# Kernel tuning notes

Hardware: AMD Instinct MI355X
Metric: run time of the kernel (lower is better)

## Reference

```python
import jax, jax.numpy as jnp
import numpy as np

N, D, E = 100000, 128, 600000  # nodes, channels, edges per subgraph


def _cos(a, b, eps=1e-8):
    # torch.nn.functional.cosine_similarity semantics (norm clamped at eps)
    na = jnp.maximum(jnp.linalg.norm(a, axis=-1), eps)
    nb = jnp.maximum(jnp.linalg.norm(b, axis=-1), eps)
    return jnp.sum(a * b, axis=-1) / (na * nb)


def _get_edge_att(x, edge_index, edge_attr):
    # utils.get_edge_att (source unavailable): edge weight modulated by
    # endpoint-feature cosine similarity.
    return edge_attr * _cos(x[edge_index[0]], x[edge_index[1]])


def _cgat(x, edge_index, edge_attr, node_mask, W, b):
    m = node_mask[:, None]
    h = jnp.where(m, x @ W.T, x)                       # lin only on masked nodes
    msg = edge_attr[:, None] * h[edge_index[0]]        # [E, D]
    ssum = jax.ops.segment_sum(msg, edge_index[1], num_segments=N)
    cnt = jax.ops.segment_sum(jnp.ones_like(edge_attr), edge_index[1], num_segments=N)
    mean = ssum / jnp.maximum(cnt, 1.0)[:, None]       # safe mean (0 for isolated nodes)
    out = jnp.where(m, mean, 0.0) + h                  # aggr only written at masked nodes
    return jnp.where(m, jax.nn.sigmoid(out + b), out)


def setup_inputs() -> dict:
    key = jax.random.key(0)
    ks = jax.random.split(key, 10)
    x = jax.random.normal(ks[0], (N, D), jnp.float32)
    edge_index_ii = jax.random.randint(ks[1], (2, E), 0, N)
    edge_attr_ii = jax.random.uniform(ks[2], (E,), jnp.float32)
    edge_index_uiu = jax.random.randint(ks[3], (2, E), 0, N)
    edge_attr_uiu = jax.random.uniform(ks[4], (E,), jnp.float32)
    node_mask_item = jnp.arange(N) < (N * 8 // 10)
    s = 1.0 / np.sqrt(D)  # torch Linear default init range
    W1_ii = jax.random.uniform(ks[5], (D, D), jnp.float32, -s, s)
    W2_ii = jax.random.uniform(ks[6], (D, D), jnp.float32, -s, s)
    W_uiu = jax.random.uniform(ks[7], (D, D), jnp.float32, -s, s)
    z = jnp.zeros((D,), jnp.float32)  # bias zero-initialized in reset_parameters
    return {
        "x": x,
        "edge_attr_ii": edge_attr_ii,
        "edge_attr_uiu": edge_attr_uiu,
        "W1_ii": W1_ii, "b1_ii": z, "W2_ii": W2_ii, "b2_ii": z,
        "W_uiu": W_uiu, "b_uiu": z,
        "edge_index_ii": edge_index_ii,
        "edge_index_uiu": edge_index_uiu,
        "node_mask_item": node_mask_item,
    }


def reference(x, edge_attr_ii, edge_attr_uiu, W1_ii, b1_ii, W2_ii, b2_ii,
              W_uiu, b_uiu, edge_index_ii, edge_index_uiu, node_mask_item):
    # item-item graph
    ea1 = _get_edge_att(x, edge_index_ii, edge_attr_ii)
    x1 = _cgat(x, edge_index_ii, ea1, node_mask_item, W1_ii, b1_ii)
    ea2 = _get_edge_att(x1, edge_index_ii, edge_attr_ii)
    x2 = _cgat(x1, edge_index_ii, ea2, node_mask_item, W2_ii, b2_ii)
    # user-item graph (cgat1_uiu applied twice in the source)
    all_mask = jnp.ones((N,), bool)
    u1 = _cgat(x2, edge_index_uiu, edge_attr_uiu, all_mask, W_uiu, b_uiu)
    u2 = _cgat(u1, edge_index_uiu, edge_attr_uiu, all_mask, W_uiu, b_uiu)
    # edge predictions on the uiu edges (the only nonzero part of edge_y_pred)
    return _cos(u2[edge_index_uiu[0]], u2[edge_index_uiu[1]])
```

## Files before the change

kernel.cpp:

```cpp
#include <hip/hip_runtime.h>
#include <cstdint>
#include <cmath>

#define D 128
#define SCAN_BS 1024

typedef __attribute__((ext_vector_type(8))) short bf16x8;
typedef __attribute__((ext_vector_type(4))) float f32x4;

__device__ __forceinline__ unsigned short f2b(float f) {
    unsigned u = __float_as_uint(f);
    return (unsigned short)((u + 0x7FFFu + ((u >> 16) & 1u)) >> 16);
}
__device__ __forceinline__ unsigned pack2(float a, float b) {
    return (unsigned)f2b(a) | ((unsigned)f2b(b) << 16);
}
__device__ __forceinline__ float blo(unsigned u) { return __uint_as_float(u << 16); }
__device__ __forceinline__ float bhi(unsigned u) { return __uint_as_float(u & 0xffff0000u); }
__device__ __forceinline__ int swzbyte(int row, int b) {
    return (row << 8) + (b ^ ((row & 7) << 4));
}

__device__ __forceinline__ unsigned fp8pk4(float a, float b, float c, float d) {
    int w = __builtin_amdgcn_cvt_pk_fp8_f32(a, b, 0, false);
    w = __builtin_amdgcn_cvt_pk_fp8_f32(c, d, w, true);
    return (unsigned)w;
}
__device__ __forceinline__ unsigned char fp8one(float v) {
    return (unsigned char)(__builtin_amdgcn_cvt_pk_fp8_f32(v, v, 0, false) & 0xff);
}
__device__ __forceinline__ void fp8up8(uint2 w, float* f) {
    auto l0 = __builtin_amdgcn_cvt_pk_f32_fp8((int)w.x, false);
    auto h0 = __builtin_amdgcn_cvt_pk_f32_fp8((int)w.x, true);
    auto l1 = __builtin_amdgcn_cvt_pk_f32_fp8((int)w.y, false);
    auto h1 = __builtin_amdgcn_cvt_pk_f32_fp8((int)w.y, true);
    f[0] = l0[0]; f[1] = l0[1]; f[2] = h0[0]; f[3] = h0[1];
    f[4] = l1[0]; f[5] = l1[1]; f[6] = h1[0]; f[7] = h1[1];
}

__global__ void mask_canon_kernel(const unsigned char* __restrict__ mraw,
                                  int* __restrict__ mout, int n) {
    int i = blockIdx.x * blockDim.x + threadIdx.x;
    if (i >= n) return;
    bool isbool = (mraw[1] | mraw[2] | mraw[3]) != 0;
    int v;
    if (isbool) v = (mraw[i] != 0);
    else        v = (((const int*)mraw)[i] != 0);
    mout[i] = v;
}

__global__ void conv_norm_kernel(const float* __restrict__ x,
                                 unsigned short* __restrict__ xb,
                                 unsigned char* __restrict__ xn8, int n) {
    int t = blockIdx.x * blockDim.x + threadIdx.x;
    int i = t >> 4, sl = t & 15;
    if (i >= n) return;
    unsigned rid = ((unsigned)i << 4) | (unsigned)sl;
    const float4* ip = (const float4*)(x + (size_t)i * D) + sl * 2;
    float4 a = ip[0], b = ip[1];
    float f[8] = {a.x, a.y, a.z, a.w, b.x, b.y, b.z, b.w};
    float acc = 0.f;
    #pragma unroll
    for (int q = 0; q < 8; q++) acc += f[q] * f[q];
    #pragma unroll
    for (int o = 8; o; o >>= 1) acc += __shfl_xor(acc, o);
    float r = 1.0f / fmaxf(sqrtf(acc), 1e-8f);
    uint4 ob;
    #pragma unroll
    for (int q = 0; q < 4; q++) (&ob.x)[q] = pack2(f[2*q], f[2*q+1]);
    ((uint4*)xb)[rid] = ob;
    uint2 o8;
    o8.x = fp8pk4(f[0]*r, f[1]*r, f[2]*r, f[3]*r);
    o8.y = fp8pk4(f[4]*r, f[5]*r, f[6]*r, f[7]*r);
    ((uint2*)xn8)[rid] = o8;
}

__global__ void w3_to_b16_kernel(const float* __restrict__ W1, const float* __restrict__ W2,
                                 const float* __restrict__ Wu,
                                 unsigned short* __restrict__ o1, unsigned short* __restrict__ o2,
                                 unsigned short* __restrict__ ou) {
    int t = blockIdx.x * blockDim.x + threadIdx.x;
    const float* src; unsigned short* dst; int b;
    if (t < 2048)      { src = W1; dst = o1; b = t; }
    else if (t < 4096) { src = W2; dst = o2; b = t - 2048; }
    else               { src = Wu; dst = ou; b = t - 4096; }
    const float4* ip = (const float4*)src + (size_t)b * 2;
    float4 a = ip[0], c = ip[1];
    uint4 o;
    o.x = pack2(a.x, a.y); o.y = pack2(a.z, a.w);
    o.z = pack2(c.x, c.y); o.w = pack2(c.z, c.w);
    ((uint4*)dst)[b] = o;
}

__global__ void count_pos2_kernel(const int* __restrict__ dstA, const int* __restrict__ dstB,
                                  int* __restrict__ tmp2, int* __restrict__ posw,
                                  int n, int e_total) {
    int t = blockIdx.x * blockDim.x + threadIdx.x;
    if (t >= 2 * e_total) return;
    int g = (t >= e_total);
    int e = t - g * e_total;
    int d = (g ? dstB : dstA)[e];
    posw[t] = atomicAdd(&tmp2[(size_t)g * n + d], 1);
}

__global__ __launch_bounds__(SCAN_BS)
void scan_block_kernel(const int* __restrict__ deg2, int* __restrict__ off2,
                       int* __restrict__ bsum2, int n) {
    __shared__ int s[SCAN_BS];
    int g = blockIdx.y;
    int gid = blockIdx.x * SCAN_BS + threadIdx.x;
    int v = (gid < n) ? deg2[(size_t)g * n + gid] : 0;
    s[threadIdx.x] = v;
    __syncthreads();
    for (int o = 1; o < SCAN_BS; o <<= 1) {
        int t = (threadIdx.x >= o) ? s[threadIdx.x - o] : 0;
        __syncthreads();
        s[threadIdx.x] += t;
        __syncthreads();
    }
    if (gid < n) off2[(size_t)g * (n + 1) + gid] = s[threadIdx.x] - v;
    if (threadIdx.x == SCAN_BS - 1) bsum2[g * 256 + blockIdx.x] = s[SCAN_BS - 1];
}

__global__ void scan_bsum_kernel(int* __restrict__ bsum2, int nb) {
    __shared__ int s[256];
    int g = blockIdx.y;
    int v = ((int)threadIdx.x < nb) ? bsum2[g * 256 + threadIdx.x] : 0;
    s[threadIdx.x] = v;
    __syncthreads();
    for (int o = 1; o < 256; o <<= 1) {
        int t = (threadIdx.x >= o) ? s[threadIdx.x - o] : 0;
        __syncthreads();
        s[threadIdx.x] += t;
        __syncthreads();
    }
    if ((int)threadIdx.x < nb) bsum2[g * 256 + threadIdx.x] = s[threadIdx.x] - v;
}

__global__ __launch_bounds__(SCAN_BS)
void add_offsets_kernel(int* __restrict__ off2, const int* __restrict__ bsum2,
                        int n, int e_total) {
    int g = blockIdx.y;
    int gid = blockIdx.x * SCAN_BS + threadIdx.x;
    if (gid < n) off2[(size_t)g * (n + 1) + gid] += bsum2[g * 256 + blockIdx.x];
    if (gid == 0) off2[(size_t)g * (n + 1) + n] = e_total;
}

__global__ void scatter_edges2_kernel(const int* __restrict__ srcA, const int* __restrict__ dstA,
                                      const float* __restrict__ aA,
                                      const int* __restrict__ srcB, const int* __restrict__ dstB,
                                      const float* __restrict__ aB,
                                      const int* __restrict__ off2, const int* __restrict__ posw,
                                      int2* __restrict__ edaA, int2* __restrict__ edaB,
                                      int n, int e_total) {
    int t = blockIdx.x * blockDim.x + threadIdx.x;
    if (t >= 2 * e_total) return;
    int g = (t >= e_total);
    int e = t - g * e_total;
    int d = (g ? dstB : dstA)[e];
    int p = off2[(size_t)g * (n + 1) + d] + posw[t];
    int2 rec;
    rec.x = (g ? srcB : srcA)[e];
    rec.y = __float_as_int((g ? aB : aA)[e]);
    (g ? edaB : edaA)[p] = rec;
}

__global__ __launch_bounds__(512)
void gemm_mfma_kernel(const unsigned short* __restrict__ xb,
                      const unsigned short* __restrict__ Wb,
                      const int* __restrict__ mask,
                      unsigned short* __restrict__ hb,
                      unsigned char* __restrict__ hb8, int n) {
    __shared__ char sXb[128 * 256];
    __shared__ char sWb[128 * 256];
    const int tid = threadIdx.x;
    const int blockRow0 = blockIdx.x * 128;

    const uint4* xg = (const uint4*)xb + (size_t)blockRow0 * 16;
    #pragma unroll
    for (int it = 0; it < 4; it++) {
        int f = tid + it * 512;
        int row = f >> 4, kc = f & 15;
        uint4 v = make_uint4(0, 0, 0, 0);
        if (blockRow0 + row < n) v = xg[f];
        *(uint4*)(sXb + swzbyte(row, kc * 16)) = v;
    }
    const uint4* wg = (const uint4*)Wb;
    #pragma unroll
    for (int it = 0; it < 4; it++) {
        int f = tid + it * 512;
        int row = f >> 4, kc = f & 15;
        *(uint4*)(sWb + swzbyte(row, kc * 16)) = wg[f];
    }
    __syncthreads();

    const int wid = tid >> 6, lane = tid & 63;
    const int lrow = lane & 15, kg = lane >> 4;
    f32x4 acc[8];
    #pragma unroll
    for (int j = 0; j < 8; j++) acc[j] = (f32x4)(0.f);

    const int arow = wid * 16 + lrow;
    #pragma unroll
    for (int kk = 0; kk < 4; kk++) {
        int kb = kk * 64 + kg * 16;
        bf16x8 af = *(const bf16x8*)(sXb + swzbyte(arow, kb));
        #pragma unroll
        for (int j = 0; j < 8; j++) {
            bf16x8 bfr = *(const bf16x8*)(sWb + swzbyte(j * 16 + lrow, kb));
            acc[j] = __builtin_amdgcn_mfma_f32_16x16x32_bf16(af, bfr, acc[j], 0, 0, 0);
        }
    }

    const int growbase = blockRow0 + wid * 16 + kg * 4;
    const int lrbase = wid * 16 + kg * 4;
    #pragma unroll
    for (int r = 0; r < 4; r++) {
        int row = growbase + r;
        if (row >= n) continue;
        bool pm = mask ? (mask[row] != 0) : true;
        int lr = lrbase + r;
        #pragma unroll
        for (int j = 0; j < 8; j++) {
            int col = j * 16 + lrow;
            float v;
            if (pm) v = acc[j][r];
            else    v = blo((unsigned)*(const unsigned short*)(sXb + (lr << 8) + ((2 * col) ^ ((lr & 7) << 4))));
            hb [(size_t)row * D + col] = f2b(v);
            hb8[(size_t)row * D + col] = fp8one(v);
        }
    }
}

__global__ __launch_bounds__(256)
void fused_agg_kernel(const unsigned short* __restrict__ hb,
                      const unsigned char* __restrict__ hb8,
                      const unsigned char* __restrict__ xn8,
                      const int2* __restrict__ eda,
                      const int* __restrict__ off,
                      const float* __restrict__ bias, const int* __restrict__ mask,
                      unsigned short* __restrict__ outb,
                      unsigned char* __restrict__ xnout8, int n) {
    int t = blockIdx.x * blockDim.x + threadIdx.x;
    int i = t >> 4, sl = t & 15;
    if (i >= n) return;
    const uint2* h8 = (const uint2*)hb8;
    const uint2* x8 = (const uint2*)xn8;
    unsigned rid = ((unsigned)i << 4) | (unsigned)sl;
    uint4 hv = ((const uint4*)hb)[rid];
    bool m = mask ? (mask[i] != 0) : true;

    float fo[8];
    if (!m) {
        #pragma unroll
        for (int q = 0; q < 4; q++) {
            unsigned u = (&hv.x)[q];
            fo[2*q] = blo(u); fo[2*q+1] = bhi(u);
        }
    } else {
        float xd[8];
        if (xn8) fp8up8(x8[rid], xd);

        int s0 = off[i], s1 = off[i + 1];
        float acc[8];
        #pragma unroll
        for (int k = 0; k < 8; k++) acc[k] = 0.f;

        int p = s0;
        while (p + 2 <= s1) {
            int2 e0 = eda[p], e1 = eda[p + 1];
            unsigned r0 = ((unsigned)e0.x << 4) | (unsigned)sl;
            unsigned r1 = ((unsigned)e1.x << 4) | (unsigned)sl;
            uint2 g0 = h8[r0], g1 = h8[r1];
            float c0 = __int_as_float(e0.y), c1 = __int_as_float(e1.y);
            if (xn8) {
                float xs0[8], xs1[8];
                fp8up8(x8[r0], xs0);
                fp8up8(x8[r1], xs1);
                float pr0 = 0.f, pr1 = 0.f;
                #pragma unroll
                for (int k = 0; k < 8; k++) {
                    pr0 += xs0[k] * xd[k];
                    pr1 += xs1[k] * xd[k];
                }
                #pragma unroll
                for (int o = 8; o; o >>= 1) {
                    pr0 += __shfl_xor(pr0, o);
                    pr1 += __shfl_xor(pr1, o);
                }
                c0 *= pr0; c1 *= pr1;
            }
            float f0[8], f1[8];
            fp8up8(g0, f0);
            fp8up8(g1, f1);
            #pragma unroll
            for (int k = 0; k < 8; k++) acc[k] += c0 * f0[k] + c1 * f1[k];
            p += 2;
        }
        if (p < s1) {
            int2 e0 = eda[p];
            unsigned r0 = ((unsigned)e0.x << 4) | (unsigned)sl;
            uint2 g0 = h8[r0];
            float c0 = __int_as_float(e0.y);
            if (xn8) {
                float xs0[8];
                fp8up8(x8[r0], xs0);
                float pr0 = 0.f;
                #pragma unroll
                for (int k = 0; k < 8; k++) pr0 += xs0[k] * xd[k];
                #pragma unroll
                for (int o = 8; o; o >>= 1) pr0 += __shfl_xor(pr0, o);
                c0 *= pr0;
            }
            float f0[8];
            fp8up8(g0, f0);
            #pragma unroll
            for (int k = 0; k < 8; k++) acc[k] += c0 * f0[k];
        }

        float inv = 1.0f / fmaxf((float)(s1 - s0), 1.0f);
        const float4* bp = (const float4*)(bias + 8 * sl);
        float4 bv0 = bp[0], bv1 = bp[1];
        float bb[8] = {bv0.x, bv0.y, bv0.z, bv0.w, bv1.x, bv1.y, bv1.z, bv1.w};
        #pragma unroll
        for (int q = 0; q < 4; q++) {
            unsigned u = (&hv.x)[q];
            float z0 = acc[2*q]   * inv + blo(u) + bb[2*q];
            float z1 = acc[2*q+1] * inv + bhi(u) + bb[2*q+1];
            fo[2*q]   = 1.0f / (1.0f + __expf(-z0));
            fo[2*q+1] = 1.0f / (1.0f + __expf(-z1));
        }
    }

    uint4 o;
    #pragma unroll
    for (int q = 0; q < 4; q++) (&o.x)[q] = pack2(fo[2*q], fo[2*q+1]);
    ((uint4*)outb)[rid] = o;

    if (xnout8) {
        float ss = 0.f;
        #pragma unroll
        for (int k = 0; k < 8; k++) ss += fo[k] * fo[k];
        #pragma unroll
        for (int o2 = 8; o2; o2 >>= 1) ss += __shfl_xor(ss, o2);
        float r = 1.0f / fmaxf(sqrtf(ss), 1e-8f);
        uint2 on;
        on.x = fp8pk4(fo[0]*r, fo[1]*r, fo[2]*r, fo[3]*r);
        on.y = fp8pk4(fo[4]*r, fo[5]*r, fo[6]*r, fo[7]*r);
        ((uint2*)xnout8)[rid] = on;
    }
}

__global__ void edge_cos_b16_kernel(const unsigned short* __restrict__ xb,
                                    const int* __restrict__ src,
                                    const int* __restrict__ dst,
                                    float* __restrict__ out, int e_total) {
    int t = blockIdx.x * blockDim.x + threadIdx.x;
    int e = t >> 4, lane = t & 15;
    if (e >= e_total) return;
    int s = src[e], d = dst[e];
    uint4 a = ((const uint4*)xb)[((unsigned)s << 4) | lane];
    uint4 b = ((const uint4*)xb)[((unsigned)d << 4) | lane];
    float sd = 0.f, ss = 0.f, dd = 0.f;
    #pragma unroll
    for (int q = 0; q < 4; q++) {
        unsigned ua = (&a.x)[q], ub = (&b.x)[q];
        float a0 = blo(ua), a1 = bhi(ua), b0 = blo(ub), b1 = bhi(ub);
        sd += a0 * b0 + a1 * b1;
        ss += a0 * a0 + a1 * a1;
        dd += b0 * b0 + b1 * b1;
    }
    #pragma unroll
    for (int o = 8; o; o >>= 1) {
        sd += __shfl_xor(sd, o, 16);
        ss += __shfl_xor(ss, o, 16);
        dd += __shfl_xor(dd, o, 16);
    }
    if (lane == 0) {
        float rs = 1.0f / fmaxf(sqrtf(ss), 1e-8f);
        float rd = 1.0f / fmaxf(sqrtf(dd), 1e-8f);
        out[e] = sd * rs * rd;
    }
}

extern "C" void kernel_launch(void* const* d_in, const int* in_sizes, int n_in,
                              void* d_out, int out_size, void* d_ws, size_t ws_size,
                              hipStream_t stream) {
    const float* x        = (const float*)d_in[0];
    const float* attr_ii  = (const float*)d_in[1];
    const float* attr_uiu = (const float*)d_in[2];
    const float* W1       = (const float*)d_in[3];
    const float* b1       = (const float*)d_in[4];
    const float* W2       = (const float*)d_in[5];
    const float* b2       = (const float*)d_in[6];
    const float* Wu       = (const float*)d_in[7];
    const float* bu       = (const float*)d_in[8];
    const int*   ei_ii    = (const int*)d_in[9];
    const int*   ei_uiu   = (const int*)d_in[10];
    const unsigned char* mraw = (const unsigned char*)d_in[11];

    const int n = in_sizes[0] / D;
    const int e = in_sizes[1];
    const size_t ND = (size_t)n * D;

    unsigned short* Ab  = (unsigned short*)d_ws;
    unsigned short* Bb0 = Ab + ND;
    unsigned short* Bb1 = Bb0 + ND;
    unsigned short* Wb1 = Bb1 + ND;
    unsigned short* Wb2 = Wb1 + 16384;
    unsigned short* Wbu = Wb2 + 16384;
    unsigned char* Ab8  = (unsigned char*)(Wbu + 16384);
    unsigned char* Xn80 = Ab8 + ND;
    unsigned char* Xn81 = Xn80 + ND;
    int2* eda_ii  = (int2*)(Xn81 + ND);
    int2* eda_uiu = eda_ii + e;
    int* maskI    = (int*)(eda_uiu + e);
    int* tmp2     = maskI + n;
    int* bsum2    = tmp2 + 2 * (size_t)n;
    int* off2     = bsum2 + 512;
    int* off_ii   = off2;
    int* off_uiu  = off2 + (n + 1);
    int* posw     = (int*)Ab;

    const int* src_ii  = ei_ii,  * dst_ii  = ei_ii + e;
    const int* src_uiu = ei_uiu, * dst_uiu = ei_uiu + e;
    float* out = (float*)d_out;

    const int nb = (n + SCAN_BS - 1) / SCAN_BS;
    const int gN16 = ((size_t)n * 16 + 255) / 256;
    const int gE16 = ((size_t)e * 16 + 255) / 256;
    const int gGemm = (n + 127) / 128;

    mask_canon_kernel<<<(n + 255) / 256, 256, 0, stream>>>(mraw, maskI, n);

    hipMemsetAsync(tmp2, 0, 2 * (size_t)n * sizeof(int), stream);
    count_pos2_kernel<<<(2 * e + 255) / 256, 256, 0, stream>>>(dst_ii, dst_uiu, tmp2, posw, n, e);
    scan_block_kernel<<<dim3(nb, 2), SCAN_BS, 0, stream>>>(tmp2, off2, bsum2, n);
    scan_bsum_kernel<<<dim3(1, 2), 256, 0, stream>>>(bsum2, nb);
    add_offsets_kernel<<<dim3(nb, 2), SCAN_BS, 0, stream>>>(off2, bsum2, n, e);
    scatter_edges2_kernel<<<(2 * e + 255) / 256, 256, 0, stream>>>(
        src_ii, dst_ii, attr_ii, src_uiu, dst_uiu, attr_uiu, off2, posw, eda_ii, eda_uiu, n, e);

    conv_norm_kernel<<<gN16, 256, 0, stream>>>(x, Bb0, Xn80, n);
    w3_to_b16_kernel<<<24, 256, 0, stream>>>(W1, W2, Wu, Wb1, Wb2, Wbu);

    gemm_mfma_kernel<<<gGemm, 512, 0, stream>>>(Bb0, Wb1, maskI, Ab, Ab8, n);
    fused_agg_kernel<<<gN16, 256, 0, stream>>>(Ab, Ab8, Xn80, eda_ii, off_ii, b1, maskI, Bb1, Xn81, n);

    gemm_mfma_kernel<<<gGemm, 512, 0, stream>>>(Bb1, Wb2, maskI, Ab, Ab8, n);
    fused_agg_kernel<<<gN16, 256, 0, stream>>>(Ab, Ab8, Xn81, eda_ii, off_ii, b2, maskI, Bb0, nullptr, n);

    gemm_mfma_kernel<<<gGemm, 512, 0, stream>>>(Bb0, Wbu, nullptr, Ab, Ab8, n);
    fused_agg_kernel<<<gN16, 256, 0, stream>>>(Ab, Ab8, nullptr, eda_uiu, off_uiu, bu, nullptr, Bb1, nullptr, n);

    gemm_mfma_kernel<<<gGemm, 512, 0, stream>>>(Bb1, Wbu, nullptr, Ab, Ab8, n);
    fused_agg_kernel<<<gN16, 256, 0, stream>>>(Ab, Ab8, nullptr, eda_uiu, off_uiu, bu, nullptr, Bb0, nullptr, n);

    edge_cos_b16_kernel<<<gE16, 256, 0, stream>>>(Bb0, src_uiu, dst_uiu, out, e);
}
```

Before: 351.9 us.

## Interleave fp8 h and normalized-x rows; fuse mask/memset into conversion kernel

Stores the fp8 transformed features and the fp8 normalized features in one interleaved 256-byte row per node. A gathered source edge then fetches both from adjacent cache lines instead of two separate arrays. The mask canonicalization, the counter memset and the fp32-to-bf16 conversion are merged into one kernel, which removes two launches. The interleaved layout doubles the stride for the uiu layers, where only the h half is read, so gather locality may suffer there.

```diff
diff --git a/kernel.cpp b/kernel.cpp
--- a/kernel.cpp
+++ b/kernel.cpp
@@ -38,24 +38,20 @@
     f[4] = l1[0]; f[5] = l1[1]; f[6] = h1[0]; f[7] = h1[1];
 }
 
-__global__ void mask_canon_kernel(const unsigned char* __restrict__ mraw,
-                                  int* __restrict__ mout, int n) {
-    int i = blockIdx.x * blockDim.x + threadIdx.x;
-    if (i >= n) return;
-    bool isbool = (mraw[1] | mraw[2] | mraw[3]) != 0;
-    int v;
-    if (isbool) v = (mraw[i] != 0);
-    else        v = (((const int*)mraw)[i] != 0);
-    mout[i] = v;
-}
-
-__global__ void conv_norm_kernel(const float* __restrict__ x,
-                                 unsigned short* __restrict__ xb,
-                                 unsigned char* __restrict__ xn8, int n) {
-    int t = blockIdx.x * blockDim.x + threadIdx.x;
+__global__ void conv_mask_zero_kernel(const float* __restrict__ x,
+                                      const unsigned char* __restrict__ mraw,
+                                      unsigned short* __restrict__ xb,
+                                      unsigned char* __restrict__ pk,
+                                      int* __restrict__ maskI,
+                                      int* __restrict__ tmp2, int n) {
+    int t = blockIdx.x * blockDim.x + threadIdx.x;
+    if (t < 2 * n) tmp2[t] = 0;
+    if (t < n) {
+        bool isbool = (mraw[1] | mraw[2] | mraw[3]) != 0;
+        maskI[t] = isbool ? (mraw[t] != 0) : (((const int*)mraw)[t] != 0);
+    }
     int i = t >> 4, sl = t & 15;
     if (i >= n) return;
-    unsigned rid = ((unsigned)i << 4) | (unsigned)sl;
     const float4* ip = (const float4*)(x + (size_t)i * D) + sl * 2;
     float4 a = ip[0], b = ip[1];
     float f[8] = {a.x, a.y, a.z, a.w, b.x, b.y, b.z, b.w};
@@ -68,11 +64,11 @@
     uint4 ob;
     #pragma unroll
     for (int q = 0; q < 4; q++) (&ob.x)[q] = pack2(f[2*q], f[2*q+1]);
-    ((uint4*)xb)[rid] = ob;
+    ((uint4*)xb)[((unsigned)i << 4) | (unsigned)sl] = ob;
     uint2 o8;
     o8.x = fp8pk4(f[0]*r, f[1]*r, f[2]*r, f[3]*r);
     o8.y = fp8pk4(f[4]*r, f[5]*r, f[6]*r, f[7]*r);
-    ((uint2*)xn8)[rid] = o8;
+    ((uint2*)pk)[(unsigned)i * 32u + 16u + (unsigned)sl] = o8;
 }
 
 __global__ void w3_to_b16_kernel(const float* __restrict__ W1, const float* __restrict__ W2,
@@ -170,7 +166,7 @@
                       const unsigned short* __restrict__ Wb,
                       const int* __restrict__ mask,
                       unsigned short* __restrict__ hb,
-                      unsigned char* __restrict__ hb8, int n) {
+                      unsigned char* __restrict__ pk, int n) {
     __shared__ char sXb[128 * 256];
     __shared__ char sWb[128 * 256];
     const int tid = threadIdx.x;
@@ -226,26 +222,25 @@
             float v;
             if (pm) v = acc[j][r];
             else    v = blo((unsigned)*(const unsigned short*)(sXb + (lr << 8) + ((2 * col) ^ ((lr & 7) << 4))));
-            hb [(size_t)row * D + col] = f2b(v);
-            hb8[(size_t)row * D + col] = fp8one(v);
+            hb[(size_t)row * D + col] = f2b(v);
+            pk[(size_t)row * 256 + col] = fp8one(v);
         }
     }
 }
 
 __global__ __launch_bounds__(256)
 void fused_agg_kernel(const unsigned short* __restrict__ hb,
-                      const unsigned char* __restrict__ hb8,
-                      const unsigned char* __restrict__ xn8,
+                      const unsigned char* __restrict__ pk,
+                      const int usecos,
                       const int2* __restrict__ eda,
                       const int* __restrict__ off,
                       const float* __restrict__ bias, const int* __restrict__ mask,
                       unsigned short* __restrict__ outb,
-                      unsigned char* __restrict__ xnout8, int n) {
+                      unsigned char* __restrict__ pknext, int n) {
     int t = blockIdx.x * blockDim.x + threadIdx.x;
     int i = t >> 4, sl = t & 15;
     if (i >= n) return;
-    const uint2* h8 = (const uint2*)hb8;
-    const uint2* x8 = (const uint2*)xn8;
+    const uint2* p2 = (const uint2*)pk;
     unsigned rid = ((unsigned)i << 4) | (unsigned)sl;
     uint4 hv = ((const uint4*)hb)[rid];
     bool m = mask ? (mask[i] != 0) : true;
@@ -259,7 +254,7 @@
         }
     } else {
         float xd[8];
-        if (xn8) fp8up8(x8[rid], xd);
+        if (usecos) fp8up8(p2[(unsigned)i * 32u + 16u + (unsigned)sl], xd);
 
         int s0 = off[i], s1 = off[i + 1];
         float acc[8];
@@ -269,14 +264,14 @@
         int p = s0;
         while (p + 2 <= s1) {
             int2 e0 = eda[p], e1 = eda[p + 1];
-            unsigned r0 = ((unsigned)e0.x << 4) | (unsigned)sl;
-            unsigned r1 = ((unsigned)e1.x << 4) | (unsigned)sl;
-            uint2 g0 = h8[r0], g1 = h8[r1];
+            unsigned r0 = (unsigned)e0.x * 32u + (unsigned)sl;
+            unsigned r1 = (unsigned)e1.x * 32u + (unsigned)sl;
+            uint2 g0 = p2[r0], g1 = p2[r1];
             float c0 = __int_as_float(e0.y), c1 = __int_as_float(e1.y);
-            if (xn8) {
+            if (usecos) {
                 float xs0[8], xs1[8];
-                fp8up8(x8[r0], xs0);
-                fp8up8(x8[r1], xs1);
+                fp8up8(p2[r0 + 16u], xs0);
+                fp8up8(p2[r1 + 16u], xs1);
                 float pr0 = 0.f, pr1 = 0.f;
                 #pragma unroll
                 for (int k = 0; k < 8; k++) {
@@ -299,12 +294,12 @@
         }
         if (p < s1) {
             int2 e0 = eda[p];
-            unsigned r0 = ((unsigned)e0.x << 4) | (unsigned)sl;
-            uint2 g0 = h8[r0];
+            unsigned r0 = (unsigned)e0.x * 32u + (unsigned)sl;
+            uint2 g0 = p2[r0];
             float c0 = __int_as_float(e0.y);
-            if (xn8) {
+            if (usecos) {
                 float xs0[8];
-                fp8up8(x8[r0], xs0);
+                fp8up8(p2[r0 + 16u], xs0);
                 float pr0 = 0.f;
                 #pragma unroll
                 for (int k = 0; k < 8; k++) pr0 += xs0[k] * xd[k];
@@ -337,7 +332,7 @@
     for (int q = 0; q < 4; q++) (&o.x)[q] = pack2(fo[2*q], fo[2*q+1]);
     ((uint4*)outb)[rid] = o;
 
-    if (xnout8) {
+    if (pknext) {
         float ss = 0.f;
         #pragma unroll
         for (int k = 0; k < 8; k++) ss += fo[k] * fo[k];
@@ -347,7 +342,7 @@
         uint2 on;
         on.x = fp8pk4(fo[0]*r, fo[1]*r, fo[2]*r, fo[3]*r);
         on.y = fp8pk4(fo[4]*r, fo[5]*r, fo[6]*r, fo[7]*r);
-        ((uint2*)xnout8)[rid] = on;
+        ((uint2*)pknext)[(unsigned)i * 32u + 16u + (unsigned)sl] = on;
     }
 }
 
@@ -409,10 +404,9 @@
     unsigned short* Wb1 = Bb1 + ND;
     unsigned short* Wb2 = Wb1 + 16384;
     unsigned short* Wbu = Wb2 + 16384;
-    unsigned char* Ab8  = (unsigned char*)(Wbu + 16384);
-    unsigned char* Xn80 = Ab8 + ND;
-    unsigned char* Xn81 = Xn80 + ND;
-    int2* eda_ii  = (int2*)(Xn81 + ND);
+    unsigned char* PK0 = (unsigned char*)(Wbu + 16384);
+    unsigned char* PK1 = PK0 + 2 * ND;
+    int2* eda_ii  = (int2*)(PK1 + 2 * ND);
     int2* eda_uiu = eda_ii + e;
     int* maskI    = (int*)(eda_uiu + e);
     int* tmp2     = maskI + n;
@@ -431,9 +425,8 @@
     const int gE16 = ((size_t)e * 16 + 255) / 256;
     const int gGemm = (n + 127) / 128;
 
-    mask_canon_kernel<<<(n + 255) / 256, 256, 0, stream>>>(mraw, maskI, n);
-
-    hipMemsetAsync(tmp2, 0, 2 * (size_t)n * sizeof(int), stream);
+    conv_mask_zero_kernel<<<gN16, 256, 0, stream>>>(x, mraw, Bb0, PK0, maskI, tmp2, n);
+
     count_pos2_kernel<<<(2 * e + 255) / 256, 256, 0, stream>>>(dst_ii, dst_uiu, tmp2, posw, n, e);
     scan_block_kernel<<<dim3(nb, 2), SCAN_BS, 0, stream>>>(tmp2, off2, bsum2, n);
     scan_bsum_kernel<<<dim3(1, 2), 256, 0, stream>>>(bsum2, nb);
@@ -441,20 +434,19 @@
     scatter_edges2_kernel<<<(2 * e + 255) / 256, 256, 0, stream>>>(
         src_ii, dst_ii, attr_ii, src_uiu, dst_uiu, attr_uiu, off2, posw, eda_ii, eda_uiu, n, e);
 
-    conv_norm_kernel<<<gN16, 256, 0, stream>>>(x, Bb0, Xn80, n);
     w3_to_b16_kernel<<<24, 256, 0, stream>>>(W1, W2, Wu, Wb1, Wb2, Wbu);
 
-    gemm_mfma_kernel<<<gGemm, 512, 0, stream>>>(Bb0, Wb1, maskI, Ab, Ab8, n);
-    fused_agg_kernel<<<gN16, 256, 0, stream>>>(Ab, Ab8, Xn80, eda_ii, off_ii, b1, maskI, Bb1, Xn81, n);
-
-    gemm_mfma_kernel<<<gGemm, 512, 0, stream>>>(Bb1, Wb2, maskI, Ab, Ab8, n);
-    fused_agg_kernel<<<gN16, 256, 0, stream>>>(Ab, Ab8, Xn81, eda_ii, off_ii, b2, maskI, Bb0, nullptr, n);
-
-    gemm_mfma_kernel<<<gGemm, 512, 0, stream>>>(Bb0, Wbu, nullptr, Ab, Ab8, n);
-    fused_agg_kernel<<<gN16, 256, 0, stream>>>(Ab, Ab8, nullptr, eda_uiu, off_uiu, bu, nullptr, Bb1, nullptr, n);
-
-    gemm_mfma_kernel<<<gGemm, 512, 0, stream>>>(Bb1, Wbu, nullptr, Ab, Ab8, n);
-    fused_agg_kernel<<<gN16, 256, 0, stream>>>(Ab, Ab8, nullptr, eda_uiu, off_uiu, bu, nullptr, Bb0, nullptr, n);
+    gemm_mfma_kernel<<<gGemm, 512, 0, stream>>>(Bb0, Wb1, maskI, Ab, PK0, n);
+    fused_agg_kernel<<<gN16, 256, 0, stream>>>(Ab, PK0, 1, eda_ii, off_ii, b1, maskI, Bb1, PK1, n);
+
+    gemm_mfma_kernel<<<gGemm, 512, 0, stream>>>(Bb1, Wb2, maskI, Ab, PK1, n);
+    fused_agg_kernel<<<gN16, 256, 0, stream>>>(Ab, PK1, 1, eda_ii, off_ii, b2, maskI, Bb0, nullptr, n);
+
+    gemm_mfma_kernel<<<gGemm, 512, 0, stream>>>(Bb0, Wbu, nullptr, Ab, PK0, n);
+    fused_agg_kernel<<<gN16, 256, 0, stream>>>(Ab, PK0, 0, eda_uiu, off_uiu, bu, nullptr, Bb1, nullptr, n);
+
+    gemm_mfma_kernel<<<gGemm, 512, 0, stream>>>(Bb1, Wbu, nullptr, Ab, PK1, n);
+    fused_agg_kernel<<<gN16, 256, 0, stream>>>(Ab, PK1, 0, eda_uiu, off_uiu, bu, nullptr, Bb0, nullptr, n);
 
     edge_cos_b16_kernel<<<gE16, 256, 0, stream>>>(Bb0, src_uiu, dst_uiu, out, e);
 }
```

Result: faster. 345.0 us (-2.0%).
